# Kernel optimization log

Measured on AMD Instinct MI355X. Metric: run time of the kernel, lower is better.

Reference implementation:

```python
import jax, jax.numpy as jnp
import numpy as np

WIN = 16; DIM = 256; HEADS = 8; B = 2; H = 256; W_ = 256
SEL = 0.25; TEMP = 1.0


def _conv(x, w, b, stride=1, pad=1, groups=1):
    y = jax.lax.conv_general_dilated(
        x, w, (stride, stride), [(pad, pad), (pad, pad)],
        dimension_numbers=('NCHW', 'OIHW', 'NCHW'), feature_group_count=groups)
    return y + b[None, :, None, None]


def _rel_pos_index(w):
    coords = np.stack(np.meshgrid(np.arange(w), np.arange(w), indexing='ij'), 0).reshape(2, -1)
    rel = (coords[:, :, None] - coords[:, None, :]).transpose(1, 2, 0) + w - 1
    return jnp.asarray(rel[:, :, 0] * (2 * w - 1) + rel[:, :, 1])


def setup_inputs():
    key = jax.random.key(0)
    ks = jax.random.split(key, 10)
    C, w = DIM, WIN
    p = lambda k, shp, s=0.02: jax.random.normal(k, shp, jnp.float32) * s
    return dict(
        x=jax.random.normal(ks[0], (B, H, W_, C), jnp.float32),
        sd_w1=p(ks[1], (4, C, 3, 3)), sd_b1=jnp.zeros((4,), jnp.float32),
        sd_w2=p(ks[2], (4, 4, w, w)), sd_b2=jnp.zeros((4,), jnp.float32),
        sd_w3=p(ks[3], (4, 4, 3, 3)), sd_b3=jnp.zeros((4,), jnp.float32),
        in_w=p(ks[4], (3 * C, C)), in_b=jnp.zeros((3 * C,), jnp.float32),
        pe_table=p(ks[5], ((2 * w - 1) ** 2, HEADS)),
        out_w=p(ks[6], (C, C)), out_b=jnp.zeros((C,), jnp.float32),
        oc_w=p(ks[7], (C, 1, 3, 3)), oc_b=jnp.zeros((C,), jnp.float32),
    )


def reference(x, sd_w1, sd_b1, sd_w2, sd_b2, sd_w3, sd_b3, in_w, in_b, pe_table, out_w, out_b, oc_w, oc_b):
    w = WIN; C = DIM; nH = HEADS; hd = C // nH
    xc = jnp.transpose(x, (0, 3, 1, 2))  # [B,C,H,W]
    Bn, _, Hh, Ww = xc.shape
    # --- sparse discriminator: per-window scores / gates / offsets ---
    sd = jax.nn.silu(_conv(xc, sd_w1, sd_b1))
    sd = jax.nn.silu(_conv(sd, sd_w2, sd_b2, stride=w, pad=0))
    sd = _conv(sd, sd_w3, sd_b3)                      # [B,4,Hw,Ww]
    scores = sd[:, 0]
    gates = jax.nn.sigmoid(sd[:, 1])
    offsets = jax.nn.sigmoid(sd[:, 2:4])
    Hw, Www = scores.shape[1], scores.shape[2]
    k = int(Hw * Www * SEL)
    # --- top-k window selection (eval: softmax, straight-through to 1) ---
    gs = jax.nn.softmax(scores.reshape(Bn, -1) / TEMP, axis=-1)
    vals, topk = jax.lax.top_k(gs, k)                 # [B,k]
    scores_delta = (jax.lax.stop_gradient(1.0 - vals) + vals).reshape(-1)
    h_idx = (topk // Www).reshape(-1)
    w_idx = (topk % Www).reshape(-1)
    b_idx = jnp.broadcast_to(jnp.arange(Bn)[:, None], (Bn, k)).reshape(-1)
    g = gates[b_idx, h_idx, w_idx]
    hard = (g > 0.5).astype(jnp.float32)
    gates_delta = jax.lax.stop_gradient(hard - g) + g
    # --- learned-offset window coordinates (trunc like .long()) ---
    h_off = (offsets[b_idx, 0, h_idx, w_idx] * w - w / 2.0).astype(jnp.int32)
    w_off = (offsets[b_idx, 1, h_idx, w_idx] * w - w / 2.0).astype(jnp.int32)
    h1 = jnp.clip(h_idx * w + h_off, 0, Hh - w)
    w1 = jnp.clip(w_idx * w + w_off, 0, Ww - w)
    # --- roi_align (aligned=False, 1 sample/bin): bilinear at half-pixel centers ---
    ar = jnp.arange(w, dtype=jnp.float32) + 0.5
    yy = jnp.clip(h1[:, None].astype(jnp.float32) + ar, 0.0, Hh - 1.0)  # [N,w]
    xx = jnp.clip(w1[:, None].astype(jnp.float32) + ar, 0.0, Ww - 1.0)
    y0 = jnp.floor(yy).astype(jnp.int32); ly = yy - y0
    x0 = jnp.floor(xx).astype(jnp.int32); lx = xx - x0
    y1p = jnp.minimum(y0 + 1, Hh - 1); x1p = jnp.minimum(x0 + 1, Ww - 1)
    bI = b_idx[:, None, None]
    gather = lambda ys, xs: xc[bI, :, ys[:, :, None], xs[:, None, :]]  # [N,w,w,C]
    wy1 = ly[:, :, None, None]; wy0 = 1.0 - wy1
    wx1 = lx[:, None, :, None]; wx0 = 1.0 - wx1
    x_before = (wy0 * wx0 * gather(y0, x0) + wy0 * wx1 * gather(y0, x1p)
                + wy1 * wx0 * gather(y1p, x0) + wy1 * wx1 * gather(y1p, x1p))
    N = x_before.shape[0]
    # --- windowed MHA with relative position bias ---
    qkv = x_before.reshape(N, w * w, C) @ in_w.T + in_b
    q, kk, v = jnp.split(qkv, 3, axis=-1)
    heads = lambda t: t.reshape(N, w * w, nH, hd).transpose(0, 2, 1, 3)
    q, kk, v = heads(q), heads(kk), heads(v)
    pe = pe_table[_rel_pos_index(w)].transpose(2, 0, 1)[None]  # [1,nH,w2,w2]
    attn = jax.nn.softmax(jnp.einsum('nhqd,nhkd->nhqk', q, kk) * hd ** (-0.5) + pe, axis=-1)
    o = jnp.einsum('nhqk,nhkd->nhqd', attn, v).transpose(0, 2, 1, 3).reshape(N, w, w, C)
    x_after = o @ out_w.T + out_b
    delta = (x_after - x_before) * (gates_delta * scores_delta)[:, None, None, None]
    delta = delta * hard[:, None, None, None]  # gate-dropped windows contribute nothing
    # --- scatter-reduce 'mean' back into the image ---
    abs_h = h1[:, None] + jnp.arange(w)
    abs_w = w1[:, None] + jnp.arange(w)
    flat = ((b_idx[:, None, None] * Hh + abs_h[:, :, None]) * Ww + abs_w[:, None, :]).reshape(-1)
    sums = jnp.zeros((Bn * Hh * Ww, C), jnp.float32).at[flat].add(delta.reshape(-1, C))
    cnts = jnp.zeros((Bn * Hh * Ww,), jnp.float32).at[flat].add(
        jnp.broadcast_to(hard[:, None, None], (N, w, w)).reshape(-1))
    mean = jnp.where(cnts[:, None] > 0, sums / jnp.maximum(cnts[:, None], 1.0), 0.0)
    xc = xc + mean.reshape(Bn, Hh, Ww, C).transpose(0, 3, 1, 2)
    out = _conv(xc, oc_w, oc_b, groups=C)  # depthwise 3x3
    return jnp.transpose(out, (0, 2, 3, 1))
```

## Files before the change

### kernel.cpp

```cpp
#include <hip/hip_runtime.h>

typedef __attribute__((ext_vector_type(8))) short short8v;
typedef __attribute__((ext_vector_type(4))) float f32x4;

#define DEV __device__ __forceinline__

DEV float sigmoidf_(float x){ return 1.0f/(1.0f+expf(-x)); }
DEV float siluf_(float x){ return x/(1.0f+expf(-x)); }
DEV ushort f2bf(float f){
  union{float f; unsigned u;} a; a.f = f;
  unsigned r = a.u + 0x7fffu + ((a.u >> 16) & 1u);
  return (ushort)(r >> 16);
}


DEV void wq_frag(const float* __restrict__ w, ushort* __restrict__ Wq,
                 int i, int nfrag){
  if (i >= nfrag) return;
  int l  = i & 63;
  int kc = (i >> 6) & 7;
  int jt = i >> 9;
  int j = jt*16 + (l & 15);
  int k = kc*32 + (l >> 4)*8;
  const float4* src = (const float4*)(w + j*256 + k);
  float4 v0 = src[0], v1 = src[1];
  union{ uint4 q; ushort u[8]; } o;
  o.u[0]=f2bf(v0.x); o.u[1]=f2bf(v0.y); o.u[2]=f2bf(v0.z); o.u[3]=f2bf(v0.w);
  o.u[4]=f2bf(v1.x); o.u[5]=f2bf(v1.y); o.u[6]=f2bf(v1.z); o.u[7]=f2bf(v1.w);
  *(uint4*)(Wq + (size_t)i*8) = o.q;
}

__global__ void k_prep(const float* __restrict__ w1, float* __restrict__ w36,
                       const float* __restrict__ in_w, ushort* __restrict__ Wq,
                       const float* __restrict__ out_w, ushort* __restrict__ Wq2,
                       const float* __restrict__ pe_table, float* __restrict__ PEf,
                       float* __restrict__ cnts){
  int bid = blockIdx.x, t = threadIdx.x;
  if (bid < 2048){
    int id = bid*256 + t;
    int h = id >> 16, q = (id>>8)&255, j = id&255;
    int ih = (q>>4) - (j>>4) + 15;
    int iw = (q&15) - (j&15) + 15;
    PEf[id] = pe_table[(ih*31+iw)*8 + h];
  } else if (bid < 2084){
    int i = (bid-2048)*256 + t;
    if (i < 9216){
      int kk = i % 9, o = (i/9) & 3, c = i / 36;
      w36[i] = w1[(o*256 + c)*9 + kk];
    }
  } else if (bid < 2180){
    wq_frag(in_w, Wq, (bid-2084)*256 + t, 24576);
  } else if (bid < 2212){
    wq_frag(out_w, Wq2, (bid-2180)*256 + t, 8192);
  } else {
    int i = (bid-2212)*256 + t;
    float4 z = make_float4(0.f,0.f,0.f,0.f);
    ((float4*)cnts)[i*2]   = z;
    ((float4*)cnts)[i*2+1] = z;
  }
}

__global__ __launch_bounds__(256) void k_c1a(const float* __restrict__ x,
    const float* __restrict__ w36, float* __restrict__ p36a, float* __restrict__ p36b){
  int pix = blockIdx.x*256 + threadIdx.x;
  int kb  = blockIdx.y;
  const float* xr = x + (size_t)pix*256 + kb*128;
  const float* wb = w36 + kb*128*36;
  float acc[36];
  #pragma unroll
  for (int j=0;j<36;++j) acc[j]=0.f;
  #pragma unroll 4
  for (int c4=0; c4<32; ++c4){
    float4 xv = *(const float4*)(xr + c4*4);
    float xs[4] = {xv.x, xv.y, xv.z, xv.w};
    #pragma unroll
    for (int e=0;e<4;++e){
      const float4* wrow = (const float4*)(wb + (size_t)(c4*4+e)*36);
      float xe = xs[e];
      #pragma unroll
      for (int jv=0;jv<9;++jv){
        float4 wv = wrow[jv];
        acc[jv*4+0] += xe*wv.x; acc[jv*4+1] += xe*wv.y;
        acc[jv*4+2] += xe*wv.z; acc[jv*4+3] += xe*wv.w;
      }
    }
  }
  float* dst = kb ? p36b : p36a;
  #pragma unroll
  for (int j=0;j<36;++j)
    dst[(size_t)j*131072 + pix] = acc[j];
}

__global__ __launch_bounds__(256) void k_c1b(const float* __restrict__ p36a,
    const float* __restrict__ p36b, const float* __restrict__ b1,
    float* __restrict__ t1){
  int pix = blockIdx.x*256 + threadIdx.x;
  int xp = pix & 255, y = (pix>>8)&255, b = pix>>16;
  float a[4] = {b1[0], b1[1], b1[2], b1[3]};
  #pragma unroll
  for (int ky=0;ky<3;++ky){
    int yy = y+ky-1; if ((unsigned)yy>=256u) continue;
    #pragma unroll
    for (int kx=0;kx<3;++kx){
      int xx = xp+kx-1; if ((unsigned)xx>=256u) continue;
      int np = (b<<16) + yy*256 + xx;
      #pragma unroll
      for (int o=0;o<4;++o){
        size_t idx = (size_t)(o*9+ky*3+kx)*131072 + np;
        a[o] += p36a[idx] + p36b[idx];
      }
    }
  }
  int base = b*262144 + y*256 + xp;
  t1[base]        = siluf_(a[0]);
  t1[base+65536]  = siluf_(a[1]);
  t1[base+131072] = siluf_(a[2]);
  t1[base+196608] = siluf_(a[3]);
}

__global__ void k_conv2(const float* __restrict__ t1, const float* __restrict__ w2,
                        const float* __restrict__ b2, float* __restrict__ t2){
  int oidx = blockIdx.x;
  int ox = oidx & 15, oy = (oidx>>4)&15, o = (oidx>>8)&3, b = oidx>>10;
  int t = threadIdx.x;
  float acc = 0.f;
  #pragma unroll
  for (int uu=0; uu<4; ++uu){
    int u = t + uu*256;
    int ic = u >> 8, ky = (u>>4)&15, kx = u&15;
    float xv = t1[(b*4+ic)*65536 + (oy*16+ky)*256 + (ox*16+kx)];
    float wv = w2[(o*4+ic)*256 + ky*16 + kx];
    acc += xv*wv;
  }
  __shared__ float red[256];
  red[t] = acc; __syncthreads();
  for (int s=128; s>0; s>>=1){ if (t<s) red[t]+=red[t+s]; __syncthreads(); }
  if (t==0) t2[oidx] = siluf_(red[0] + b2[o]);
}

__global__ void k_sel(const float* __restrict__ t2, const float* __restrict__ w3,
                      const float* __restrict__ b3, int* __restrict__ desc){
  int b = blockIdx.x, t = threadIdx.x;
  __shared__ float sd[1024];
  #pragma unroll
  for (int oo=0; oo<4; ++oo){
    int idx = t + oo*256;
    int o = idx >> 8, oy = (idx>>4)&15, ox = idx&15;
    float acc = b3[o];
    for (int ic=0; ic<4; ++ic){
      const float* src = t2 + (b*4+ic)*256;
      const float* ww  = w3 + (o*4+ic)*9;
      #pragma unroll
      for (int ky=0; ky<3; ++ky){
        int yy = oy + ky - 1; if ((unsigned)yy >= 16u) continue;
        #pragma unroll
        for (int kx=0; kx<3; ++kx){
          int xx = ox + kx - 1; if ((unsigned)xx >= 16u) continue;
          acc += src[yy*16+xx] * ww[ky*3+kx];
        }
      }
    }
    sd[idx] = acc;
  }
  __syncthreads();
  float st = sd[t];
  int rank = 0;
  for (int j=0;j<256;++j){
    float sj = sd[j];
    rank += (sj > st) || (sj == st && j < t);
  }
  if (rank < 64){
    float g = sigmoidf_(sd[256 + t]);
    int hard = (g > 0.5f) ? 1 : 0;
    float offh = sigmoidf_(sd[512 + t]) * 16.0f - 8.0f;
    float offw = sigmoidf_(sd[768 + t]) * 16.0f - 8.0f;
    int hoff = (int)offh, woff = (int)offw;
    int h1 = min(max((t>>4)*16 + hoff, 0), 240);
    int w1 = min(max((t&15)*16 + woff, 0), 240);
    ((int4*)desc)[b*64 + rank] = make_int4(h1, w1, hard, 0);
  }
}

__global__ __launch_bounds__(256) void k_xb(const float* __restrict__ x,
    const int* __restrict__ desc, float* __restrict__ XBf, ushort* __restrict__ XBh){
  int wi = blockIdx.x;
  int4 d = ((const int4*)desc)[wi];
  if (!d.z) return;
  int b = wi >> 6;
  int ty = blockIdx.y;
  int tid = threadIdx.x;
  int tx = tid >> 4;
  int cl = (tid & 15) * 4;
  float yyf = fminf((float)(d.x + ty) + 0.5f, 255.0f);
  int y0 = (int)yyf; float ly = yyf - (float)y0; int y1 = min(y0+1, 255);
  float xxf = fminf((float)(d.y + tx) + 0.5f, 255.0f);
  int x0 = (int)xxf; float lx = xxf - (float)x0; int x1 = min(x0+1, 255);
  float w00=(1.f-ly)*(1.f-lx), w01=(1.f-ly)*lx, w10=ly*(1.f-lx), w11=ly*lx;
  const float* p00 = x + ((b*256+y0)*256 + x0)*256;
  const float* p01 = x + ((b*256+y0)*256 + x1)*256;
  const float* p10 = x + ((b*256+y1)*256 + x0)*256;
  const float* p11 = x + ((b*256+y1)*256 + x1)*256;
  size_t tokoff = ((size_t)(wi*256 + ty*16 + tx))*256;
  float* dst = XBf + tokoff;
  ushort* dsth = XBh + tokoff;
  #pragma unroll
  for (int u=0; u<4; ++u){
    int c = cl + u*64;
    float4 A = *(const float4*)(p00+c);
    float4 Bv= *(const float4*)(p01+c);
    float4 Cv= *(const float4*)(p10+c);
    float4 Dv= *(const float4*)(p11+c);
    float4 r;
    r.x = w00*A.x + w01*Bv.x + w10*Cv.x + w11*Dv.x;
    r.y = w00*A.y + w01*Bv.y + w10*Cv.y + w11*Dv.y;
    r.z = w00*A.z + w01*Bv.z + w10*Cv.z + w11*Dv.z;
    r.w = w00*A.w + w01*Bv.w + w10*Cv.w + w11*Dv.w;
    *(float4*)(dst + c) = r;
    *(ushort4*)(dsth + c) = make_ushort4(f2bf(r.x), f2bf(r.y), f2bf(r.z), f2bf(r.w));
  }
}

__global__ __launch_bounds__(256) void k_qkv(const ushort* __restrict__ XBh,
    const ushort* __restrict__ Wq, const float* __restrict__ in_b,
    const int* __restrict__ desc, ushort* __restrict__ Qs,
    ushort* __restrict__ Kb, ushort* __restrict__ Vb){
  int wi = blockIdx.x;
  if (((const int4*)desc)[wi].z == 0) return;
  int t0 = blockIdx.y * 32;
  __shared__ __align__(16) ushort Xs[32*264];
  int tid = threadIdx.x;
  const ushort* Ab = XBh + (size_t)(wi*256 + t0)*256;
  #pragma unroll
  for (int it = 0; it < 4; ++it){
    int i = tid + it*256;
    int row = i >> 5, k8 = (i & 31) * 8;
    *(uint4*)(&Xs[row*264 + k8]) = *(const uint4*)(Ab + row*256 + k8);
  }
  __syncthreads();
  int w = tid >> 6, l = tid & 63;
  int lr = l & 15, lg = l >> 4;
  f32x4 acc[2][12];
  #pragma unroll
  for (int a=0;a<2;++a)
    #pragma unroll
    for (int j=0;j<12;++j) acc[a][j] = (f32x4){0.f,0.f,0.f,0.f};
  for (int kc = 0; kc < 8; ++kc){
    short8v xf0 = *(const short8v*)(&Xs[lr*264       + kc*32 + lg*8]);
    short8v xf1 = *(const short8v*)(&Xs[(16+lr)*264 + kc*32 + lg*8]);
    #pragma unroll
    for (int jt = 0; jt < 12; ++jt){
      short8v wf = *(const short8v*)(Wq + ((size_t)((w*12 + jt)*8 + kc)*64 + l)*8);
      acc[0][jt] = __builtin_amdgcn_mfma_f32_16x16x32_bf16(xf0, wf, acc[0][jt], 0, 0, 0);
      acc[1][jt] = __builtin_amdgcn_mfma_f32_16x16x32_bf16(xf1, wf, acc[1][jt], 0, 0, 0);
    }
  }
  #pragma unroll
  for (int ts=0; ts<2; ++ts)
    #pragma unroll
    for (int jt=0; jt<12; ++jt){
      int j = w*192 + jt*16 + lr;
      #pragma unroll
      for (int r=0; r<4; ++r){
        int t = t0 + ts*16 + lg*4 + r;
        float val = acc[ts][jt][r] + in_b[j];
        if (j < 256){
          Qs[((size_t)(wi*256 + t))*256 + j] = f2bf(val * 0.17677669529663687f);
        } else if (j < 512){
          int jq = j - 256;
          Kb[((size_t)(wi*8 + (jq>>5))*256 + t)*32 + (jq&31)] = f2bf(val);
        } else {
          int jq = j - 512;
          Vb[((size_t)(wi*8 + (jq>>5))*256 + t)*32 + (jq&31)] = f2bf(val);
        }
      }
    }
}

__global__ __launch_bounds__(256,2) void k_attn(const ushort* __restrict__ Qs,
    const ushort* __restrict__ Kb, const ushort* __restrict__ Vb,
    const float* __restrict__ PEf, const int* __restrict__ desc,
    ushort* __restrict__ Ob){
  int wi = blockIdx.x, h = blockIdx.y;
  if (((const int4*)desc)[wi].z == 0) return;
  __shared__ __align__(16) ushort Ks[256*40];
  __shared__ __align__(16) ushort Vt[32*264];
  __shared__ __align__(16) ushort Pb[4][16*40];
  int tid = threadIdx.x;
  {
    const uint4* src = (const uint4*)(Kb + (size_t)((wi*8+h)*256 + tid)*32);
    uint4 a = src[0], b = src[1], c = src[2], d = src[3];
    *(uint4*)(&Ks[tid*40 +  0]) = a;
    *(uint4*)(&Ks[tid*40 +  8]) = b;
    *(uint4*)(&Ks[tid*40 + 16]) = c;
    *(uint4*)(&Ks[tid*40 + 24]) = d;
  }
  {
    const uint4* src = (const uint4*)(Vb + (size_t)((wi*8+h)*256 + tid)*32);
    #pragma unroll
    for (int c4=0; c4<4; ++c4){
      union{uint4 v; ushort u[8];} uu; uu.v = src[c4];
      #pragma unroll
      for (int e=0;e<8;++e) Vt[(c4*8+e)*264 + tid] = uu.u[e];
    }
  }
  __syncthreads();
  int w = tid >> 6, l = tid & 63;
  int lg = l >> 4, lr = l & 15;
  const float* PEh = PEf + h*65536;
  for (int s_i = 0; s_i < 4; ++s_i){
    int q0 = (w*4 + s_i)*16;
    short8v qf = *(const short8v*)(Qs + ((size_t)(wi*256 + q0 + lr))*256 + h*32 + lg*8);
    f32x4 sfr[16];
    #pragma unroll
    for (int jt=0; jt<16; ++jt){
      f32x4 c;
      #pragma unroll
      for (int r=0;r<4;++r) c[r] = PEh[(q0 + lg*4 + r)*256 + jt*16 + lr];
      short8v kf = *(const short8v*)(&Ks[(jt*16 + lr)*40 + lg*8]);
      sfr[jt] = __builtin_amdgcn_mfma_f32_16x16x32_bf16(qf, kf, c, 0, 0, 0);
    }
    float mx[4] = {-1e30f,-1e30f,-1e30f,-1e30f};
    #pragma unroll
    for (int jt=0;jt<16;++jt)
      #pragma unroll
      for (int r=0;r<4;++r) mx[r] = fmaxf(mx[r], sfr[jt][r]);
    #pragma unroll
    for (int m_=1; m_<16; m_<<=1){
      #pragma unroll
      for (int r=0;r<4;++r) mx[r] = fmaxf(mx[r], __shfl_xor(mx[r], m_));
    }
    float sm[4] = {0.f,0.f,0.f,0.f};
    #pragma unroll
    for (int jt=0;jt<16;++jt)
      #pragma unroll
      for (int r=0;r<4;++r){
        float p = __expf(sfr[jt][r] - mx[r]);
        sfr[jt][r] = p; sm[r] += p;
      }
    #pragma unroll
    for (int m_=1; m_<16; m_<<=1){
      #pragma unroll
      for (int r=0;r<4;++r) sm[r] += __shfl_xor(sm[r], m_);
    }
    f32x4 oa0 = {0.f,0.f,0.f,0.f}, oa1 = {0.f,0.f,0.f,0.f};
    ushort* pb = Pb[w];
    #pragma unroll
    for (int kc=0; kc<8; ++kc){
      #pragma unroll
      for (int t2=0;t2<2;++t2)
        #pragma unroll
        for (int r=0;r<4;++r)
          pb[(lg*4+r)*40 + t2*16 + lr] = f2bf(sfr[kc*2+t2][r]);
      short8v pf = *(const short8v*)(&pb[lr*40 + lg*8]);
      short8v v0 = *(const short8v*)(&Vt[lr*264 + kc*32 + lg*8]);
      short8v v1 = *(const short8v*)(&Vt[(16+lr)*264 + kc*32 + lg*8]);
      oa0 = __builtin_amdgcn_mfma_f32_16x16x32_bf16(pf, v0, oa0, 0, 0, 0);
      oa1 = __builtin_amdgcn_mfma_f32_16x16x32_bf16(pf, v1, oa1, 0, 0, 0);
    }
    #pragma unroll
    for (int r=0;r<4;++r){
      float inv = 1.0f / sm[r];
      size_t obase = ((size_t)(wi*256 + q0 + lg*4 + r))*256 + h*32;
      Ob[obase + lr]      = f2bf(oa0[r] * inv);
      Ob[obase + 16 + lr] = f2bf(oa1[r] * inv);
    }
  }
}

__global__ void k_zero(const int* __restrict__ desc, float* __restrict__ sums,
                       float* __restrict__ cnts){
  int wi = blockIdx.x;
  int4 d = ((const int4*)desc)[wi];
  if (!d.z) return;
  int b = wi >> 6;
  int t = threadIdx.x;
  int pix = (b*256 + d.x + (t>>4))*256 + d.y + (t&15);
  float4* p = (float4*)(sums + (size_t)pix*256);
  #pragma unroll 8
  for (int c=0;c<64;++c) p[c] = make_float4(0.f,0.f,0.f,0.f);
  atomicAdd(&cnts[pix], 1.0f);
}

__global__ __launch_bounds__(256) void k_oproj(const ushort* __restrict__ Ob,
    const ushort* __restrict__ Wq2, const float* __restrict__ out_b,
    const float* __restrict__ XBf, const int* __restrict__ desc,
    float* __restrict__ sums){
  int wi = blockIdx.x;
  int4 dsc = ((const int4*)desc)[wi];
  if (!dsc.z) return;
  int t0 = blockIdx.y * 32;
  __shared__ __align__(16) ushort Os[32*264];
  int tid = threadIdx.x;
  for (int i = tid; i < 1024; i += 256){
    int row = i >> 5, k8 = (i & 31) * 8;
    uint4 vv = *(const uint4*)(Ob + (size_t)(wi*256 + t0 + row)*256 + k8);
    *(uint4*)(&Os[row*264 + k8]) = vv;
  }
  __syncthreads();
  int w = tid >> 6, l = tid & 63;
  int lr = l & 15, lg = l >> 4;
  f32x4 acc[2][4];
  #pragma unroll
  for (int a=0;a<2;++a)
    #pragma unroll
    for (int j=0;j<4;++j) acc[a][j] = (f32x4){0.f,0.f,0.f,0.f};
  for (int kc = 0; kc < 8; ++kc){
    short8v of0 = *(const short8v*)(&Os[lr*264       + kc*32 + lg*8]);
    short8v of1 = *(const short8v*)(&Os[(16+lr)*264 + kc*32 + lg*8]);
    #pragma unroll
    for (int jt = 0; jt < 4; ++jt){
      short8v wf = *(const short8v*)(Wq2 + ((size_t)((w*4 + jt)*8 + kc)*64 + l)*8);
      acc[0][jt] = __builtin_amdgcn_mfma_f32_16x16x32_bf16(of0, wf, acc[0][jt], 0, 0, 0);
      acc[1][jt] = __builtin_amdgcn_mfma_f32_16x16x32_bf16(of1, wf, acc[1][jt], 0, 0, 0);
    }
  }
  int b = wi >> 6;
  #pragma unroll
  for (int ts=0; ts<2; ++ts)
    #pragma unroll
    for (int jt=0; jt<4; ++jt){
      int j = w*64 + jt*16 + lr;
      #pragma unroll
      for (int r=0; r<4; ++r){
        int t = t0 + ts*16 + lg*4 + r;
        int pix = (b*256 + dsc.x + (t>>4))*256 + dsc.y + (t&15);
        float delta = acc[ts][jt][r] + out_b[j] - XBf[((size_t)(wi*256 + t))*256 + j];
        atomicAdd(&sums[(size_t)pix*256 + j], delta);
      }
    }
}

__global__ __launch_bounds__(256) void k_final(const float* __restrict__ x,
    const float* __restrict__ sums, const float* __restrict__ cnts,
    const float* __restrict__ ocw, const float* __restrict__ ocb,
    float* __restrict__ out){
  int x0 = blockIdx.x * 16;
  int y0 = blockIdx.y * 2;
  int b  = blockIdx.z;
  int c  = threadIdx.x;
  __shared__ float wl[2304];
  __shared__ float bl[256];
  __shared__ float invc[72];
  __shared__ int   anyc;
  if (threadIdx.x == 0) anyc = 0;
  for (int i = threadIdx.x; i < 2304; i += 256) wl[i] = ocw[i];
  bl[c] = ocb[c];
  __syncthreads();
  if (threadIdx.x < 72){
    int rr = threadIdx.x / 18, cc = threadIdx.x % 18;
    int yy = y0 + rr - 1, xx = x0 + cc - 1;
    float iv = 0.f;
    if ((unsigned)yy < 256u && (unsigned)xx < 256u){
      float cv = cnts[(b*256+yy)*256 + xx];
      if (cv > 0.f) iv = 1.0f / cv;
    }
    invc[threadIdx.x] = iv;
    if (iv != 0.f) anyc = 1;
  }
  float v[4][18];
  #pragma unroll
  for (int rr=0; rr<4; ++rr){
    int yy = y0 + rr - 1;
    int yc = min(max(yy, 0), 255);
    float ym = ((unsigned)yy < 256u) ? 1.f : 0.f;
    const float* rowb = x + ((size_t)((b*256+yc)*256))*256 + c;
    #pragma unroll
    for (int cc=0; cc<18; ++cc){
      int xx = x0 + cc - 1;
      int xc = min(max(xx, 0), 255);
      float m = ((unsigned)xx < 256u) ? ym : 0.f;
      v[rr][cc] = rowb[(size_t)xc*256] * m;
    }
  }
  #pragma unroll
  for (int rr=0; rr<4; ++rr)
    #pragma unroll
    for (int cc=0; cc<18; ++cc)
      asm volatile("" : "+v"(v[rr][cc]));
  __syncthreads();
  if (anyc){
    #pragma unroll
    for (int rr=0; rr<4; ++rr){
      int yy = y0 + rr - 1;
      int yc = min(max(yy, 0), 255);
      #pragma unroll
      for (int cc=0; cc<18; ++cc){
        int xx = x0 + cc - 1;
        int xc = min(max(xx, 0), 255);
        float iv = invc[rr*18 + cc];
        const float* bp = (iv != 0.f) ? sums : x;
        size_t idx = ((size_t)((b*256+yc)*256 + xc))*256 + c;
        v[rr][cc] += bp[idx] * iv;
      }
    }
  }
  float w0=wl[c*9+0], w1=wl[c*9+1], w2=wl[c*9+2],
        w3=wl[c*9+3], w4=wl[c*9+4], w5=wl[c*9+5],
        w6=wl[c*9+6], w7=wl[c*9+7], w8=wl[c*9+8];
  float bias = bl[c];
  #pragma unroll
  for (int r=0; r<2; ++r){
    size_t obase = ((size_t)((b*256+y0+r)*256 + x0))*256 + c;
    #pragma unroll
    for (int oc=0; oc<16; ++oc){
      float acc = bias
        + w0*v[r  ][oc] + w1*v[r  ][oc+1] + w2*v[r  ][oc+2]
        + w3*v[r+1][oc] + w4*v[r+1][oc+1] + w5*v[r+1][oc+2]
        + w6*v[r+2][oc] + w7*v[r+2][oc+1] + w8*v[r+2][oc+2];
      out[obase + (size_t)oc*256] = acc;
    }
  }
}

extern "C" void kernel_launch(void* const* d_in, const int* in_sizes, int n_in,
                              void* d_out, int out_size, void* d_ws, size_t ws_size,
                              hipStream_t stream){
  const float* x     = (const float*)d_in[0];
  const float* sd_w1 = (const float*)d_in[1];
  const float* sd_b1 = (const float*)d_in[2];
  const float* sd_w2 = (const float*)d_in[3];
  const float* sd_b2 = (const float*)d_in[4];
  const float* sd_w3 = (const float*)d_in[5];
  const float* sd_b3 = (const float*)d_in[6];
  const float* in_w  = (const float*)d_in[7];
  const float* in_b  = (const float*)d_in[8];
  const float* pe_t  = (const float*)d_in[9];
  const float* out_w = (const float*)d_in[10];
  const float* out_b = (const float*)d_in[11];
  const float* oc_w  = (const float*)d_in[12];
  const float* oc_b  = (const float*)d_in[13];
  float* out = (float*)d_out;
  char* ws = (char*)d_ws;
  if (ws_size < 204003328ULL) return;

  float*  w36 = (float*)(ws + 0);
  float*  t1  = (float*)(ws + 36864);
  float*  t2  = (float*)(ws + 2134016);
  int*    desc= (int*)  (ws + 2150400);
  ushort* Wq  = (ushort*)(ws + 2152448);
  ushort* Wq2 = (ushort*)(ws + 2545664);
  float*  XBf = (float*)(ws + 2676736);
  float*  p36a= (float*)(ws + 2676736);
  float*  p36b= (float*)(ws + 21551104);
  ushort* Ob  = (ushort*)(ws + 36231168);
  float*  sums= (float*)(ws + 69261312);
  ushort* Qs  = (ushort*)(ws + 69261312);
  ushort* Kb  = (ushort*)(ws + 86038528);
  ushort* Vb  = (ushort*)(ws + 102815744);
  float*  PEf = (float*)(ws + 119592960);
  ushort* XBh = (ushort*)(ws + 121690112);
  float*  cnts= (float*)(ws + 203479040);

  k_prep <<<2276, 256, 0, stream>>>(sd_w1, w36, in_w, Wq, out_w, Wq2,
                                    pe_t, PEf, cnts);
  k_c1a  <<<dim3(512,2), 256, 0, stream>>>(x, w36, p36a, p36b);
  k_c1b  <<<512,  256, 0, stream>>>(p36a, p36b, sd_b1, t1);
  k_conv2<<<2048, 256, 0, stream>>>(t1, sd_w2, sd_b2, t2);
  k_sel  <<<2,    256, 0, stream>>>(t2, sd_w3, sd_b3, desc);
  k_xb   <<<dim3(128,16), 256, 0, stream>>>(x, desc, XBf, XBh);
  k_qkv  <<<dim3(128,8),  256, 0, stream>>>(XBh, Wq, in_b, desc, Qs, Kb, Vb);
  k_attn <<<dim3(128,8),  256, 0, stream>>>(Qs, Kb, Vb, PEf, desc, Ob);
  k_zero <<<128,  256, 0, stream>>>(desc, sums, cnts);
  k_oproj<<<dim3(128,8),  256, 0, stream>>>(Ob, Wq2, out_b, XBf, desc, sums);
  k_final<<<dim3(16,128,2),256, 0, stream>>>(x, sums, cnts, oc_w, oc_b, out);
}
```

Before: 267.8 us.

## Fuse conv1 epilogue with stride-16 conv2 and transpose positional bias table

Merges the conv1 reduction/SiLU kernel with the window-level stride-16 conv2. Each block now covers one 16x16 window and does the 4x4 output-channel dot product plus a shared-memory tree reduction, so the t1 intermediate is never written to or read from global memory and one launch is removed. Separately, the precomputed positional-bias table is stored transposed so the attention kernel can load its MFMA accumulator init as a single contiguous float4 instead of four strided scalars. The cost is a larger 4-way shared reduction per block.

```diff
diff --git a/kernel.cpp b/kernel.cpp
--- a/kernel.cpp
+++ b/kernel.cpp
@@ -38,7 +38,7 @@
   int bid = blockIdx.x, t = threadIdx.x;
   if (bid < 2048){
     int id = bid*256 + t;
-    int h = id >> 16, q = (id>>8)&255, j = id&255;
+    int h = id >> 16, j = (id>>8)&255, q = id&255;
     int ih = (q>>4) - (j>>4) + 15;
     int iw = (q&15) - (j&15) + 15;
     PEf[id] = pe_table[(ih*31+iw)*8 + h];
@@ -91,51 +91,55 @@
     dst[(size_t)j*131072 + pix] = acc[j];
 }
 
-__global__ __launch_bounds__(256) void k_c1b(const float* __restrict__ p36a,
+__global__ __launch_bounds__(256) void k_c1bc2(const float* __restrict__ p36a,
     const float* __restrict__ p36b, const float* __restrict__ b1,
-    float* __restrict__ t1){
-  int pix = blockIdx.x*256 + threadIdx.x;
-  int xp = pix & 255, y = (pix>>8)&255, b = pix>>16;
+    const float* __restrict__ w2, const float* __restrict__ b2,
+    float* __restrict__ t2){
+  int blk = blockIdx.x;
+  int b = blk >> 8, oy = (blk>>4)&15, ox = blk&15;
+  int t = threadIdx.x;
+  int ky = t >> 4, kx = t & 15;
+  int y = oy*16 + ky, xp = ox*16 + kx;
   float a[4] = {b1[0], b1[1], b1[2], b1[3]};
   #pragma unroll
-  for (int ky=0;ky<3;++ky){
-    int yy = y+ky-1; if ((unsigned)yy>=256u) continue;
-    #pragma unroll
-    for (int kx=0;kx<3;++kx){
-      int xx = xp+kx-1; if ((unsigned)xx>=256u) continue;
+  for (int k2=0;k2<3;++k2){
+    int yy = y+k2-1; if ((unsigned)yy>=256u) continue;
+    #pragma unroll
+    for (int k3=0;k3<3;++k3){
+      int xx = xp+k3-1; if ((unsigned)xx>=256u) continue;
       int np = (b<<16) + yy*256 + xx;
       #pragma unroll
       for (int o=0;o<4;++o){
-        size_t idx = (size_t)(o*9+ky*3+kx)*131072 + np;
+        size_t idx = (size_t)(o*9+k2*3+k3)*131072 + np;
         a[o] += p36a[idx] + p36b[idx];
       }
     }
   }
-  int base = b*262144 + y*256 + xp;
-  t1[base]        = siluf_(a[0]);
-  t1[base+65536]  = siluf_(a[1]);
-  t1[base+131072] = siluf_(a[2]);
-  t1[base+196608] = siluf_(a[3]);
-}
-
-__global__ void k_conv2(const float* __restrict__ t1, const float* __restrict__ w2,
-                        const float* __restrict__ b2, float* __restrict__ t2){
-  int oidx = blockIdx.x;
-  int ox = oidx & 15, oy = (oidx>>4)&15, o = (oidx>>8)&3, b = oidx>>10;
-  int t = threadIdx.x;
-  float acc = 0.f;
-  #pragma unroll
-  for (int uu=0; uu<4; ++uu){
-    int u = t + uu*256;
-    int ic = u >> 8, ky = (u>>4)&15, kx = u&15;
-    float xv = t1[(b*4+ic)*65536 + (oy*16+ky)*256 + (ox*16+kx)];
-    float wv = w2[(o*4+ic)*256 + ky*16 + kx];
-    acc += xv*wv;
-  }
-  __shared__ float red[256];
-  red[t] = acc; __syncthreads();
-  for (int s=128; s>0; s>>=1){ if (t<s) red[t]+=red[t+s]; __syncthreads(); }
-  if (t==0) t2[oidx] = siluf_(red[0] + b2[o]);
+  float s[4];
+  #pragma unroll
+  for (int o=0;o<4;++o) s[o] = siluf_(a[o]);
+  __shared__ float red[1024];
+  #pragma unroll
+  for (int o=0;o<4;++o){
+    float acc = 0.f;
+    #pragma unroll
+    for (int ic=0;ic<4;++ic)
+      acc += s[ic] * w2[(o*4+ic)*256 + t];
+    red[o*256 + t] = acc;
+  }
+  __syncthreads();
+  for (int st=128; st>0; st>>=1){
+    if (t < st){
+      #pragma unroll
+      for (int o=0;o<4;++o) red[o*256+t] += red[o*256+t+st];
+    }
+    __syncthreads();
+  }
+  if (t == 0){
+    #pragma unroll
+    for (int o=0;o<4;++o)
+      t2[(b*4+o)*256 + oy*16 + ox] = siluf_(red[o*256] + b2[o]);
+  }
 }
 
 __global__ void k_sel(const float* __restrict__ t2, const float* __restrict__ w3,
@@ -313,11 +317,9 @@
     f32x4 sfr[16];
     #pragma unroll
     for (int jt=0; jt<16; ++jt){
-      f32x4 c;
-      #pragma unroll
-      for (int r=0;r<4;++r) c[r] = PEh[(q0 + lg*4 + r)*256 + jt*16 + lr];
+      f32x4 cinit = *(const f32x4*)(PEh + (size_t)(jt*16 + lr)*256 + q0 + lg*4);
       short8v kf = *(const short8v*)(&Ks[(jt*16 + lr)*40 + lg*8]);
-      sfr[jt] = __builtin_amdgcn_mfma_f32_16x16x32_bf16(qf, kf, c, 0, 0, 0);
+      sfr[jt] = __builtin_amdgcn_mfma_f32_16x16x32_bf16(qf, kf, cinit, 0, 0, 0);
     }
     float mx[4] = {-1e30f,-1e30f,-1e30f,-1e30f};
     #pragma unroll
@@ -534,7 +536,6 @@
   if (ws_size < 204003328ULL) return;
 
   float*  w36 = (float*)(ws + 0);
-  float*  t1  = (float*)(ws + 36864);
   float*  t2  = (float*)(ws + 2134016);
   int*    desc= (int*)  (ws + 2150400);
   ushort* Wq  = (ushort*)(ws + 2152448);
@@ -554,8 +555,7 @@
   k_prep <<<2276, 256, 0, stream>>>(sd_w1, w36, in_w, Wq, out_w, Wq2,
                                     pe_t, PEf, cnts);
   k_c1a  <<<dim3(512,2), 256, 0, stream>>>(x, w36, p36a, p36b);
-  k_c1b  <<<512,  256, 0, stream>>>(p36a, p36b, sd_b1, t1);
-  k_conv2<<<2048, 256, 0, stream>>>(t1, sd_w2, sd_b2, t2);
+  k_c1bc2<<<512,  256, 0, stream>>>(p36a, p36b, sd_b1, sd_w2, sd_b2, t2);
   k_sel  <<<2,    256, 0, stream>>>(t2, sd_w3, sd_b3, desc);
   k_xb   <<<dim3(128,16), 256, 0, stream>>>(x, desc, XBf, XBh);
   k_qkv  <<<dim3(128,8),  256, 0, stream>>>(XBh, Wq, in_b, desc, Qs, Kb, Vb);
```

Result: slower. 279.4 us (+4.3%).
